# Optimization experiments

Measured on AMD Instinct MI355X. Metric: run time of the kernel, lower is better.

The kernel has to match this reference:

```python
import jax, jax.numpy as jnp
import numpy as np

D = 512; H = 8; HD = D // H; L = 6; QD = 16; MAXLEN = 1000

def _pos_encoding(max_len, d):
    pos = jnp.arange(max_len, dtype=jnp.float32)[:, None]
    div = jnp.exp(jnp.arange(0, d, 2, dtype=jnp.float32) * (-np.log(10000.0) / d))
    pe = jnp.zeros((max_len, d), jnp.float32)
    pe = pe.at[:, 0::2].set(jnp.sin(pos * div))
    pe = pe.at[:, 1::2].set(jnp.cos(pos * div))
    return pe

def _quantum(x, W, b, qwr, qwi, sg, em, mb):
    # QuantumInspiredLayer: classical tanh branch + quantum branch fused by sigmoid gate
    classical = jnp.tanh(x @ W + b)
    qs = x @ sg                          # (B,S,QD) real superposition amplitudes
    ev_r = qs @ qwr                      # complex evolution, real/imag parts kept separate
    ev_i = qs @ qwi
    en_r = ev_r @ em                     # entanglement (real matrix)
    en_i = ev_i @ em
    probs = en_r ** 2 + en_i ** 2        # |entangled|^2, (B,S,QD)
    qout = probs @ mb                    # measurement, (B,S,D)
    fw = jax.nn.sigmoid(jnp.mean(probs, axis=-1, keepdims=True))  # (B,S,1)
    return fw * qout + (1.0 - fw) * classical, probs

def _layer(x, p):
    (Wq, bq, Wk, bk, Wv, bv, Wo, bo,
     qW, qb, qr, qi, qsg, qem, qmb,
     kW, kb, kr, ki, ksg, kem, kmb, g, beta) = p
    B, S, _ = x.shape
    Q = x @ Wq + bq
    K = x @ Wk + bk
    Vv = x @ Wv + bv
    Qq, qp = _quantum(x, qW, qb, qr, qi, qsg, qem, qmb)
    Kq, kp = _quantum(x, kW, kb, kr, ki, ksg, kem, kmb)
    Qf = (0.7 * Q + 0.3 * Qq).reshape(B, S, H, HD).transpose(0, 2, 1, 3)  # (B,H,S,hd)
    Kf = (0.7 * K + 0.3 * Kq).reshape(B, S, H, HD).transpose(0, 2, 1, 3)
    Vh = Vv.reshape(B, S, H, HD).transpose(0, 2, 1, 3)
    scores = jnp.einsum('bhid,bhjd->bhij', Qf, Kf) / np.sqrt(HD).astype(np.float32)
    interf = jnp.einsum('biq,bjq->bij', qp, kp)   # quantum interference term (B,S,S)
    scores = scores + 0.1 * interf[:, None]       # broadcast over heads
    attn = jax.nn.softmax(scores, axis=-1)        # dropout=eval mode (identity)
    ctx = jnp.einsum('bhij,bhjd->bhid', attn, Vh).transpose(0, 2, 1, 3).reshape(B, S, D)
    y = ctx @ Wo + bo + x                         # residual, then LayerNorm
    mu = jnp.mean(y, axis=-1, keepdims=True)
    var = jnp.mean((y - mu) ** 2, axis=-1, keepdims=True)
    y = (y - mu) / jnp.sqrt(var + 1e-5) * g + beta
    return y, attn

def setup_inputs() -> dict:
    key = jax.random.key(0)
    ks = iter(jax.random.split(key, 64))
    def rn(shape, s=0.02):
        return (jax.random.normal(next(ks), shape) * s).astype(jnp.float32)
    B, S, V = 4, 512, 32000
    inp = {
        'text_input': jax.random.randint(next(ks), (B, S), 0, V),
        'visual_input': rn((B, 2048), 1.0),
        'temporal_input': rn((B, 64), 1.0),
        'embed': rn((V, D)),
        'Wvis': rn((2048, D)), 'bvis': jnp.zeros((D,), jnp.float32),
        'Wtemp': rn((64, D)), 'btemp': jnp.zeros((D,), jnp.float32),
        'Wq': rn((L, D, D)), 'bq': jnp.zeros((L, D), jnp.float32),
        'Wk': rn((L, D, D)), 'bk': jnp.zeros((L, D), jnp.float32),
        'Wv': rn((L, D, D)), 'bv': jnp.zeros((L, D), jnp.float32),
        'Wo': rn((L, D, D)), 'bo': jnp.zeros((L, D), jnp.float32),
        'qW': rn((L, D, D)), 'qb': jnp.zeros((L, D), jnp.float32),
        'q_qwr': rn((L, QD, QD), 0.05), 'q_qwi': rn((L, QD, QD), 0.05),
        'q_sg': rn((L, D, QD), 0.05), 'q_em': rn((L, QD, QD), 0.05), 'q_mb': rn((L, QD, D), 0.05),
        'kW': rn((L, D, D)), 'kb': jnp.zeros((L, D), jnp.float32),
        'k_qwr': rn((L, QD, QD), 0.05), 'k_qwi': rn((L, QD, QD), 0.05),
        'k_sg': rn((L, D, QD), 0.05), 'k_em': rn((L, QD, QD), 0.05), 'k_mb': rn((L, QD, D), 0.05),
        'ln_g': jnp.ones((L, D), jnp.float32), 'ln_b': jnp.zeros((L, D), jnp.float32),
        'Ws': rn((D, 64)), 'bs_': jnp.zeros((64,), jnp.float32),
        'Wd': rn((D, 5)), 'bd': jnp.zeros((5,), jnp.float32),
        'We': rn((D, 1)), 'be': jnp.zeros((1,), jnp.float32),
    }
    return inp

def reference(text_input, visual_input, temporal_input, embed, Wvis, bvis, Wtemp, btemp,
              Wq, bq, Wk, bk, Wv, bv, Wo, bo,
              qW, qb, q_qwr, q_qwi, q_sg, q_em, q_mb,
              kW, kb, k_qwr, k_qwi, k_sg, k_em, k_mb,
              ln_g, ln_b, Ws, bs_, Wd, bd, We, be):
    B, S = text_input.shape
    x = (embed[text_input]
         + (visual_input @ Wvis + bvis)[:, None, :]
         + (temporal_input @ Wtemp + btemp)[:, None, :])
    x = x + _pos_encoding(MAXLEN, D)[None, :S, :]
    attns = []
    for l in range(L):
        p = (Wq[l], bq[l], Wk[l], bk[l], Wv[l], bv[l], Wo[l], bo[l],
             qW[l], qb[l], q_qwr[l], q_qwi[l], q_sg[l], q_em[l], q_mb[l],
             kW[l], kb[l], k_qwr[l], k_qwi[l], k_sg[l], k_em[l], k_mb[l],
             ln_g[l], ln_b[l])
        x, a = _layer(x, p)
        attns.append(a)
    pooled = jnp.mean(x, axis=1)  # no attention_mask -> simple mean pool
    skill = jax.nn.sigmoid(pooled @ Ws + bs_)
    diff = jax.nn.softmax(pooled @ Wd + bd, axis=-1)
    eng = jax.nn.sigmoid(pooled @ We + be)
    return skill, diff, eng, x, jnp.stack(attns)
```

## Files before the change

kernel.cpp:

```cpp
#include <hip/hip_runtime.h>
#include <hip/hip_bf16.h>

typedef __attribute__((ext_vector_type(4))) float f32x4;
typedef __attribute__((ext_vector_type(8))) short s16x8;

__device__ __forceinline__ unsigned short f2b(float f) {
  unsigned int u = __float_as_uint(f);
  unsigned int r = (u + 0x7FFFu + ((u >> 16) & 1u)) >> 16;
  return (unsigned short)r;
}
__device__ __forceinline__ float b2f(unsigned short h) {
  return __uint_as_float(((unsigned int)h) << 16);
}
__device__ __forceinline__ void gload16(const void* g, void* l) {
  __builtin_amdgcn_global_load_lds(
      (const __attribute__((address_space(1))) void*)g,
      (__attribute__((address_space(3))) void*)l, 16, 0, 0);
}

enum { MODE_BF16 = 0, MODE_VT = 1, MODE_Y = 2 };
struct OutSpec { void* ptr; int mode; };
struct Outs5 { OutSpec o[5]; };
struct Ptr6 { const float* p[6]; };

template<int BM, int BN, int WGM, int WGN>
__global__ __launch_bounds__(256) void gemm_nt(
    const unsigned short* __restrict__ A, int lda, long long strideA,
    const unsigned short* __restrict__ Bm, int ldb, long long strideB,
    const float* __restrict__ biasBase, int biasStride, int perZ,
    Outs5 outs, const float* __restrict__ resid, int K)
{
  constexpr int BK = 32;
  constexpr int WM = BM / WGM, WN = BN / WGN;
  constexpr int WR = WM / 16, WC = WN / 16;
  constexpr int CHA = BM * BK / 8;
  constexpr int CHB = BN * BK / 8;
  __shared__ unsigned short lds_a[2][BM * BK];
  __shared__ unsigned short lds_b[2][BN * BK];
  const int z = blockIdx.z;
  const int tid = threadIdx.x;
  const int wave = tid >> 6, lane = tid & 63;
  const int l16 = lane & 15, lhi = lane >> 4;
  const int wm = (wave / WGN) * WM, wn = (wave % WGN) * WN;
  const int m0 = blockIdx.x * BM, n0 = blockIdx.y * BN;
  const unsigned short* Ap = A + (long long)z * strideA;
  const unsigned short* Bp = Bm + (long long)z * strideB;

  auto stage = [&](int buf, int k0) {
#pragma unroll
    for (int p = 0; p < CHA / 256; ++p) {
      int t = p * 256 + tid;
      gload16(Ap + (long long)(m0 + (t >> 2)) * lda + k0 + (t & 3) * 8, &lds_a[buf][t * 8]);
    }
    if constexpr (CHA % 256) {
      if (tid < CHA % 256) {
        int t = (CHA / 256) * 256 + tid;
        gload16(Ap + (long long)(m0 + (t >> 2)) * lda + k0 + (t & 3) * 8, &lds_a[buf][t * 8]);
      }
    }
#pragma unroll
    for (int p = 0; p < CHB / 256; ++p) {
      int t = p * 256 + tid;
      gload16(Bp + (long long)(n0 + (t >> 2)) * ldb + k0 + (t & 3) * 8, &lds_b[buf][t * 8]);
    }
    if constexpr (CHB % 256) {
      if (tid < CHB % 256) {
        int t = (CHB / 256) * 256 + tid;
        gload16(Bp + (long long)(n0 + (t >> 2)) * ldb + k0 + (t & 3) * 8, &lds_b[buf][t * 8]);
      }
    }
  };

  f32x4 acc[WR][WC];
#pragma unroll
  for (int r = 0; r < WR; ++r)
#pragma unroll
    for (int c = 0; c < WC; ++c) { f32x4 zz = {0.f, 0.f, 0.f, 0.f}; acc[r][c] = zz; }

  stage(0, 0);
  __syncthreads();
  int cur = 0;
  for (int k0 = 0; k0 < K; k0 += BK) {
    if (k0 + BK < K) stage(cur ^ 1, k0 + BK);
    s16x8 af[WR], bfv[WC];
#pragma unroll
    for (int r = 0; r < WR; ++r)
      af[r] = *(const s16x8*)&lds_a[cur][(wm + r * 16 + l16) * BK + lhi * 8];
#pragma unroll
    for (int c = 0; c < WC; ++c)
      bfv[c] = *(const s16x8*)&lds_b[cur][(wn + c * 16 + l16) * BK + lhi * 8];
#pragma unroll
    for (int r = 0; r < WR; ++r)
#pragma unroll
      for (int c = 0; c < WC; ++c)
        acc[r][c] = __builtin_amdgcn_mfma_f32_16x16x32_bf16(af[r], bfv[c], acc[r][c], 0, 0, 0);
    __syncthreads();
    cur ^= 1;
  }

  OutSpec spec = perZ ? outs.o[z] : outs.o[0];
  const float* bias = biasBase ? (biasBase + (long long)z * biasStride) : nullptr;
#pragma unroll
  for (int r = 0; r < WR; ++r) {
#pragma unroll
    for (int c = 0; c < WC; ++c) {
      int n = n0 + wn + c * 16 + l16;
      int rb = m0 + wm + r * 16 + lhi * 4;
      float bv = bias ? bias[n] : 0.f;
      float vv[4];
#pragma unroll
      for (int j = 0; j < 4; ++j) vv[j] = acc[r][c][j] + bv;
      if (spec.mode == MODE_BF16) {
#pragma unroll
        for (int j = 0; j < 4; ++j)
          ((unsigned short*)spec.ptr)[(long long)(rb + j) * 512 + n] = f2b(vv[j]);
      } else if (spec.mode == MODE_VT) {
        int b = rb >> 9, s = rb & 511;
        ushort4 pk;
        pk.x = f2b(vv[0]); pk.y = f2b(vv[1]); pk.z = f2b(vv[2]); pk.w = f2b(vv[3]);
        *(ushort4*)&((unsigned short*)spec.ptr)[
            (((long long)(b * 8 + (n >> 6))) * 64 + (n & 63)) * 512 + s] = pk;
      } else {
#pragma unroll
        for (int j = 0; j < 4; ++j)
          ((float*)spec.ptr)[(long long)(rb + j) * 512 + n] =
              vv[j] + resid[(long long)(rb + j) * 512 + n];
      }
    }
  }
}

__global__ __launch_bounds__(256, 1) void fused_attn(
    const unsigned short* __restrict__ Qe, const unsigned short* __restrict__ Ke,
    const unsigned short* __restrict__ Vt, float* __restrict__ attn,
    unsigned short* __restrict__ ctx)
{
  __shared__ unsigned short lds[55296];
  const int z = blockIdx.x, rb = blockIdx.y;
  const int m0 = rb * 64;
  const int b = z >> 3, h = z & 7;
  const int tid = threadIdx.x;
  const int w = tid >> 6, lane = tid & 63;
  const int l16 = lane & 15, lhi = lane >> 4;
  const int rx3 = l16 & 3, rx7 = l16 & 7;

#pragma unroll
  for (int p = 0; p < 3; ++p) {
    int t = p * 256 + tid;
    int row = t / 12, c = t % 12;
    gload16(Qe + ((long long)(z * 512 + m0 + row)) * 96 + (c ^ (row & 3)) * 8, &lds[t * 8]);
  }
#pragma unroll
  for (int p = 0; p < 24; ++p) {
    int t = p * 256 + tid;
    int row = t / 12, c = t % 12;
    gload16(Ke + ((long long)(z * 512 + row)) * 96 + (c ^ (row & 3)) * 8, &lds[6144 + t * 8]);
  }
  __syncthreads();

  const unsigned short* Qs = lds;
  const unsigned short* Ks = lds + 6144;
  s16x8 aq[3];
#pragma unroll
  for (int kk = 0; kk < 3; ++kk)
    aq[kk] = *(const s16x8*)&Qs[(w * 16 + l16) * 96 + (kk * 4 + (lhi ^ rx3)) * 8];
  f32x4 acc[32];
#pragma unroll
  for (int c = 0; c < 32; ++c) { f32x4 zz = {0.f, 0.f, 0.f, 0.f}; acc[c] = zz; }
#pragma unroll
  for (int c = 0; c < 32; ++c) {
#pragma unroll
    for (int kk = 0; kk < 3; ++kk) {
      s16x8 bf = *(const s16x8*)&Ks[(c * 16 + l16) * 96 + (kk * 4 + (lhi ^ rx3)) * 8];
      acc[c] = __builtin_amdgcn_mfma_f32_16x16x32_bf16(aq[kk], bf, acc[c], 0, 0, 0);
    }
  }

  float inv[4];
#pragma unroll
  for (int j = 0; j < 4; ++j) {
    float mx = acc[0][j];
#pragma unroll
    for (int c = 1; c < 32; ++c) mx = fmaxf(mx, acc[c][j]);
    mx = fmaxf(mx, __shfl_xor(mx, 1));
    mx = fmaxf(mx, __shfl_xor(mx, 2));
    mx = fmaxf(mx, __shfl_xor(mx, 4));
    mx = fmaxf(mx, __shfl_xor(mx, 8));
    float sum = 0.f;
#pragma unroll
    for (int c = 0; c < 32; ++c) { float e = __expf(acc[c][j] - mx); acc[c][j] = e; sum += e; }
    sum += __shfl_xor(sum, 1);
    sum += __shfl_xor(sum, 2);
    sum += __shfl_xor(sum, 4);
    sum += __shfl_xor(sum, 8);
    inv[j] = 1.f / sum;
  }
  __syncthreads();

#pragma unroll
  for (int p = 0; p < 8; ++p) {
    int t = p * 256 + tid;
    int row = t >> 5, c = t & 31;
    gload16(Vt + (long long)z * 32768 + row * 512 + (c ^ (row & 7)) * 8, &lds[32768 + t * 8]);
  }
  unsigned short* S = lds;
  {
    float* ap = attn + (long long)z * 262144;
#pragma unroll
    for (int j = 0; j < 4; ++j) {
      int row_l = w * 16 + lhi * 4 + j;
      int rs = row_l & 7;
      float* arow = ap + (long long)(m0 + row_l) * 512;
      unsigned short* srow = S + row_l * 512;
#pragma unroll
      for (int c = 0; c < 32; ++c) {
        float p = acc[c][j] * inv[j];
        int col = c * 16 + l16;
        arow[col] = p;
        srow[((col >> 3) ^ rs) * 8 + (col & 7)] = f2b(p);
      }
    }
  }
  __syncthreads();

  const unsigned short* Vl = lds + 32768;
  f32x4 acc2[4];
#pragma unroll
  for (int c2 = 0; c2 < 4; ++c2) { f32x4 zz = {0.f, 0.f, 0.f, 0.f}; acc2[c2] = zz; }
  const int qrow = w * 16 + l16;
#pragma unroll
  for (int kk = 0; kk < 8; ++kk) {
    s16x8 a = *(const s16x8*)&S[qrow * 512 + ((kk * 4 + lhi) ^ rx7) * 8];
#pragma unroll
    for (int c2 = 0; c2 < 4; ++c2) {
      s16x8 bf = *(const s16x8*)&Vl[(c2 * 16 + l16) * 256 + ((kk * 4 + lhi) ^ rx7) * 8];
      acc2[c2] = __builtin_amdgcn_mfma_f32_16x16x32_bf16(a, bf, acc2[c2], 0, 0, 0);
    }
  }
  __syncthreads();
#pragma unroll
  for (int p = 0; p < 8; ++p) {
    int t = p * 256 + tid;
    int row = t >> 5, c = t & 31;
    gload16(Vt + (long long)z * 32768 + row * 512 + 256 + (c ^ (row & 7)) * 8,
            &lds[32768 + t * 8]);
  }
  __syncthreads();
#pragma unroll
  for (int kk = 8; kk < 16; ++kk) {
    s16x8 a = *(const s16x8*)&S[qrow * 512 + ((kk * 4 + lhi) ^ rx7) * 8];
#pragma unroll
    for (int c2 = 0; c2 < 4; ++c2) {
      s16x8 bf = *(const s16x8*)&Vl[(c2 * 16 + l16) * 256 + (((kk - 8) * 4 + lhi) ^ rx7) * 8];
      acc2[c2] = __builtin_amdgcn_mfma_f32_16x16x32_bf16(a, bf, acc2[c2], 0, 0, 0);
    }
  }
#pragma unroll
  for (int c2 = 0; c2 < 4; ++c2) {
#pragma unroll
    for (int j = 0; j < 4; ++j) {
      int row_g = m0 + w * 16 + lhi * 4 + j;
      ctx[((long long)(b * 512 + row_g)) * 512 + h * 64 + c2 * 16 + l16] = f2b(acc2[c2][j]);
    }
  }
}

__global__ __launch_bounds__(256) void wt_k(Ptr6 srcs, unsigned short* __restrict__ wt) {
  __shared__ float tile[32][33];
  int zz = blockIdx.z;
  int l = zz / 6, mat = zz % 6;
  const float* src = srcs.p[mat] + (long long)l * 262144;
  int tx = threadIdx.x, ty = threadIdx.y;
  int n0 = blockIdx.x * 32, k0 = blockIdx.y * 32;
#pragma unroll
  for (int r = 0; r < 4; ++r)
    tile[ty + r * 8][tx] = src[(long long)(k0 + ty + r * 8) * 512 + n0 + tx];
  __syncthreads();
#pragma unroll
  for (int r = 0; r < 4; ++r)
    wt[(long long)zz * 262144 + (long long)(n0 + ty + r * 8) * 512 + k0 + tx] =
        f2b(tile[tx][ty + r * 8]);
}

__global__ __launch_bounds__(256) void prep_k(Ptr6 biases,
    const float* __restrict__ qwr, const float* __restrict__ qwi, const float* __restrict__ qem,
    const float* __restrict__ kwr, const float* __restrict__ kwi, const float* __restrict__ kem,
    float* __restrict__ biasPacked, float* __restrict__ ArAi) {
  int l = blockIdx.x, t = threadIdx.x;
  for (int m = 0; m < 6; ++m)
    for (int d = t; d < 512; d += 256)
      biasPacked[(l * 6 + m) * 512 + d] = biases.p[m][l * 512 + d];
  int i = t >> 4, j = t & 15;
  const float* em0 = qem + l * 256;
  float ar = 0.f, ai = 0.f;
  for (int tt = 0; tt < 16; ++tt) {
    ar += qwr[l * 256 + i * 16 + tt] * em0[tt * 16 + j];
    ai += qwi[l * 256 + i * 16 + tt] * em0[tt * 16 + j];
  }
  ArAi[(l * 4 + 0) * 256 + t] = ar;
  ArAi[(l * 4 + 1) * 256 + t] = ai;
  const float* em1 = kem + l * 256;
  ar = 0.f; ai = 0.f;
  for (int tt = 0; tt < 16; ++tt) {
    ar += kwr[l * 256 + i * 16 + tt] * em1[tt * 16 + j];
    ai += kwi[l * 256 + i * 16 + tt] * em1[tt * 16 + j];
  }
  ArAi[(l * 4 + 2) * 256 + t] = ar;
  ArAi[(l * 4 + 3) * 256 + t] = ai;
}

__global__ __launch_bounds__(512) void vispart_k(const float* __restrict__ vis,
    const float* __restrict__ Wvis, float* __restrict__ part) {
  int b = blockIdx.x, chunk = blockIdx.y, d = threadIdx.x;
  float acc = 0.f;
  for (int k = chunk * 64; k < chunk * 64 + 64; ++k)
    acc += vis[b * 2048 + k] * Wvis[(long long)k * 512 + d];
  part[(b * 32 + chunk) * 512 + d] = acc;
}
__global__ __launch_bounds__(512) void projsum_k(const float* __restrict__ part,
    const float* __restrict__ bvis, const float* __restrict__ temporal,
    const float* __restrict__ Wtemp, const float* __restrict__ btemp, float* __restrict__ proj) {
  int b = blockIdx.x, d = threadIdx.x;
  float acc = bvis[d] + btemp[d];
  for (int c = 0; c < 32; ++c) acc += part[(b * 32 + c) * 512 + d];
  for (int k = 0; k < 64; ++k) acc += temporal[b * 64 + k] * Wtemp[k * 512 + d];
  proj[b * 512 + d] = acc;
}

__global__ __launch_bounds__(512) void embed_k(const int* __restrict__ text,
    const float* __restrict__ emb, const float* __restrict__ proj,
    float* __restrict__ x, unsigned short* __restrict__ xb) {
  int row = blockIdx.x;
  int b = row >> 9, s = row & 511;
  int d = threadIdx.x;
  int tok = text[row];
  float v = emb[(long long)tok * 512 + d] + proj[b * 512 + d];
  float fr = __expf((float)((d >> 1) << 1) * (-9.2103403719761836f / 512.f));
  float ang = (float)s * fr;
  v += (d & 1) ? cosf(ang) : sinf(ang);
  x[(long long)row * 512 + d] = v;
  xb[(long long)row * 512 + d] = f2b(v);
}

__global__ __launch_bounds__(64) void quantum_k(const unsigned short* __restrict__ xb,
    const float* __restrict__ sg_q, const float* __restrict__ sg_k,
    const float* __restrict__ ArAiL, float* __restrict__ qp, float* __restrict__ kp,
    float* __restrict__ fwq, float* __restrict__ fwk) {
  int row = blockIdx.x, side = blockIdx.y, lane = threadIdx.x;
  const float* sg = side ? sg_k : sg_q;
  const float* Ar = ArAiL + side * 512;
  const float* Ai = Ar + 256;
  float acc[16];
#pragma unroll
  for (int j = 0; j < 16; ++j) acc[j] = 0.f;
  s16x8 xv8 = *(const s16x8*)(xb + (long long)row * 512 + lane * 8);
#pragma unroll
  for (int e = 0; e < 8; ++e) {
    float xv = b2f((unsigned short)xv8[e]);
    const float* sgr = sg + (lane * 8 + e) * 16;
#pragma unroll
    for (int j = 0; j < 16; ++j) acc[j] += xv * sgr[j];
  }
#pragma unroll
  for (int s = 32; s; s >>= 1)
#pragma unroll
    for (int j = 0; j < 16; ++j) acc[j] += __shfl_xor(acc[j], s);
  int j = lane & 15;
  float tr = 0.f, ti = 0.f;
#pragma unroll
  for (int t = 0; t < 16; ++t) {
    tr += acc[t] * Ar[t * 16 + j];
    ti += acc[t] * Ai[t * 16 + j];
  }
  float p = tr * tr + ti * ti;
  float ps = p;
#pragma unroll
  for (int s = 1; s < 16; s <<= 1) ps += __shfl_xor(ps, s);
  if (lane < 16) (side ? kp : qp)[row * 16 + lane] = p;
  if (lane == 0) (side ? fwk : fwq)[row] = 1.f / (1.f + __expf(-ps * (1.f / 16.f)));
}

struct FuseP {
  const unsigned short* lin; const unsigned short* cl; const float* qp; const float* fw;
  const float* mb; unsigned short* ext; float sA, sB;
};
struct Fuse2 { FuseP s[2]; };
__global__ __launch_bounds__(512) void fuse_k(Fuse2 fp) {
  FuseP P = fp.s[blockIdx.y];
  int row = blockIdx.x;
  int b = row >> 9, i = row & 511;
  int d = threadIdx.x;
  const float* qpr = P.qp + row * 16;
  float fwv = P.fw[row];
  float qout = 0.f;
#pragma unroll
  for (int t = 0; t < 16; ++t) qout += qpr[t] * P.mb[t * 512 + d];
  float qq = fwv * qout + (1.f - fwv) * tanhf(b2f(P.cl[(long long)row * 512 + d]));
  float val = (0.7f * b2f(P.lin[(long long)row * 512 + d]) + 0.3f * qq) * P.sA;
  int h = d >> 6, dd = d & 63;
  P.ext[(((long long)(b * 8 + h)) * 512 + i) * 96 + dd] = f2b(val);
  if (d < 128) {
    int h2 = d >> 4, j = d & 15;
    P.ext[(((long long)(b * 8 + h2)) * 512 + i) * 96 + 64 + j] = f2b(P.sB * qpr[j]);
  } else if (d < 256) {
    int t2 = d - 128;
    int h2 = t2 >> 4, j = t2 & 15;
    P.ext[(((long long)(b * 8 + h2)) * 512 + i) * 96 + 80 + j] = 0;
  }
}

__global__ __launch_bounds__(256) void ln_k(const float* __restrict__ y,
    const float* __restrict__ g, const float* __restrict__ be,
    float* __restrict__ xo, unsigned short* __restrict__ xb, float* __restrict__ xo2) {
  int wv = threadIdx.x >> 6, lane = threadIdx.x & 63;
  long long row = (long long)blockIdx.x * 4 + wv;
  const float* yr = y + row * 512 + lane * 8;
  f32x4 a = *(const f32x4*)yr, b = *(const f32x4*)(yr + 4);
  float s = a[0] + a[1] + a[2] + a[3] + b[0] + b[1] + b[2] + b[3];
#pragma unroll
  for (int m = 32; m; m >>= 1) s += __shfl_xor(s, m);
  float mu = s * (1.f / 512.f);
  float d[8], vs = 0.f;
#pragma unroll
  for (int j = 0; j < 4; ++j) { d[j] = a[j] - mu; vs += d[j] * d[j]; }
#pragma unroll
  for (int j = 0; j < 4; ++j) { d[4 + j] = b[j] - mu; vs += d[4 + j] * d[4 + j]; }
#pragma unroll
  for (int m = 32; m; m >>= 1) vs += __shfl_xor(vs, m);
  float rstd = rsqrtf(vs * (1.f / 512.f) + 1e-5f);
  f32x4 g0 = *(const f32x4*)(g + lane * 8), g1 = *(const f32x4*)(g + lane * 8 + 4);
  f32x4 b0 = *(const f32x4*)(be + lane * 8), b1 = *(const f32x4*)(be + lane * 8 + 4);
  f32x4 o0, o1; s16x8 ob;
#pragma unroll
  for (int j = 0; j < 4; ++j) { o0[j] = d[j] * rstd * g0[j] + b0[j]; ob[j] = (short)f2b(o0[j]); }
#pragma unroll
  for (int j = 0; j < 4; ++j) { o1[j] = d[4 + j] * rstd * g1[j] + b1[j]; ob[4 + j] = (short)f2b(o1[j]); }
  float* xr = xo + row * 512 + lane * 8;
  *(f32x4*)xr = o0; *(f32x4*)(xr + 4) = o1;
  *(s16x8*)(xb + row * 512 + lane * 8) = ob;
  if (xo2) {
    float* x2 = xo2 + row * 512 + lane * 8;
    *(f32x4*)x2 = o0; *(f32x4*)(x2 + 4) = o1;
  }
}

__global__ __launch_bounds__(512) void poolpart_k(const float* __restrict__ x,
                                                   float* __restrict__ part) {
  int b = blockIdx.x, ch = blockIdx.y, d = threadIdx.x;
  float s = 0.f;
  for (int r = 0; r < 64; ++r) s += x[((long long)(b * 512 + ch * 64 + r)) * 512 + d];
  part[(b * 8 + ch) * 512 + d] = s;
}
__global__ __launch_bounds__(512) void head_k(const float* __restrict__ part,
    const float* __restrict__ Ws, const float* __restrict__ bs,
    const float* __restrict__ Wd, const float* __restrict__ bd,
    const float* __restrict__ We, const float* __restrict__ be, float* __restrict__ out) {
  __shared__ float pooled[512];
  __shared__ float dl[5];
  int b = blockIdx.x, d = threadIdx.x;
  float s = 0.f;
  for (int t = 0; t < 8; ++t) s += part[(b * 8 + t) * 512 + d];
  pooled[d] = s * (1.f / 512.f);
  __syncthreads();
  if (d < 64) {
    float a = bs[d];
    for (int t = 0; t < 512; ++t) a += pooled[t] * Ws[t * 64 + d];
    out[b * 64 + d] = 1.f / (1.f + __expf(-a));
  } else if (d < 69) {
    int j = d - 64;
    float a = bd[j];
    for (int t = 0; t < 512; ++t) a += pooled[t] * Wd[t * 5 + j];
    dl[j] = a;
  } else if (d == 69) {
    float a = be[0];
    for (int t = 0; t < 512; ++t) a += pooled[t] * We[t];
    out[276 + b] = 1.f / (1.f + __expf(-a));
  }
  __syncthreads();
  if (d < 5) {
    float mx = dl[0];
    for (int j = 1; j < 5; ++j) mx = fmaxf(mx, dl[j]);
    float sm = 0.f;
    for (int j = 0; j < 5; ++j) sm += __expf(dl[j] - mx);
    out[256 + b * 5 + d] = __expf(dl[d] - mx) / sm;
  }
}

extern "C" void kernel_launch(void* const* d_in, const int* in_sizes, int n_in,
                              void* d_out, int out_size, void* d_ws, size_t ws_size,
                              hipStream_t stream) {
  (void)in_sizes; (void)n_in; (void)out_size; (void)ws_size;
  const int*   text     = (const int*)  d_in[0];
  const float* visual   = (const float*)d_in[1];
  const float* temporal = (const float*)d_in[2];
  const float* embedw   = (const float*)d_in[3];
  const float* Wvis  = (const float*)d_in[4];  const float* bvis  = (const float*)d_in[5];
  const float* Wtemp = (const float*)d_in[6];  const float* btemp = (const float*)d_in[7];
  const float* Wq = (const float*)d_in[8];   const float* bq = (const float*)d_in[9];
  const float* Wk = (const float*)d_in[10];  const float* bk = (const float*)d_in[11];
  const float* Wv = (const float*)d_in[12];  const float* bv = (const float*)d_in[13];
  const float* Wo = (const float*)d_in[14];  const float* bo = (const float*)d_in[15];
  const float* qW = (const float*)d_in[16];  const float* qb = (const float*)d_in[17];
  const float* q_qwr = (const float*)d_in[18]; const float* q_qwi = (const float*)d_in[19];
  const float* q_sg  = (const float*)d_in[20]; const float* q_em  = (const float*)d_in[21];
  const float* q_mb  = (const float*)d_in[22];
  const float* kW = (const float*)d_in[23];  const float* kb = (const float*)d_in[24];
  const float* k_qwr = (const float*)d_in[25]; const float* k_qwi = (const float*)d_in[26];
  const float* k_sg  = (const float*)d_in[27]; const float* k_em  = (const float*)d_in[28];
  const float* k_mb  = (const float*)d_in[29];
  const float* ln_g = (const float*)d_in[30]; const float* ln_b = (const float*)d_in[31];
  const float* Ws = (const float*)d_in[32];  const float* bs_ = (const float*)d_in[33];
  const float* Wd = (const float*)d_in[34];  const float* bd = (const float*)d_in[35];
  const float* We = (const float*)d_in[36];  const float* be = (const float*)d_in[37];
  float* out = (float*)d_out;

  char* w = (char*)d_ws;
  auto alloc = [&](size_t bytes) {
    char* p = w;
    w += (bytes + 255) & ~(size_t)255;
    return p;
  };
  float* ws_x   = (float*)alloc(2048ll * 512 * 4);
  unsigned short* ws_xb = (unsigned short*)alloc(2048ll * 512 * 2);
  unsigned short* ws_Wt = (unsigned short*)alloc(36ll * 262144 * 2);
  float* ws_bias = (float*)alloc(6ll * 6 * 512 * 4);
  float* ws_ArAi = (float*)alloc(6ll * 1024 * 4);
  float* ws_proj = (float*)alloc(4ll * 512 * 4);
  float* ws_vp   = (float*)alloc(4ll * 32 * 512 * 4);
  unsigned short* ws_Q  = (unsigned short*)alloc(2048ll * 512 * 2);
  unsigned short* ws_K  = (unsigned short*)alloc(2048ll * 512 * 2);
  unsigned short* ws_Cq = (unsigned short*)alloc(2048ll * 512 * 2);
  unsigned short* ws_Ck = (unsigned short*)alloc(2048ll * 512 * 2);
  float* ws_qp   = (float*)alloc(2048ll * 16 * 4);
  float* ws_kp   = (float*)alloc(2048ll * 16 * 4);
  float* ws_fwq  = (float*)alloc(2048ll * 4);
  float* ws_fwk  = (float*)alloc(2048ll * 4);
  unsigned short* ws_Vt   = (unsigned short*)alloc(2048ll * 512 * 2);
  unsigned short* ws_Qext = (unsigned short*)alloc(4ll * 8 * 512 * 96 * 2);
  unsigned short* ws_Kext = (unsigned short*)alloc(4ll * 8 * 512 * 96 * 2);
  unsigned short* ws_ctx  = (unsigned short*)alloc(2048ll * 512 * 2);
  float* ws_y    = (float*)alloc(2048ll * 512 * 4);

  Ptr6 wsrc = {{Wq, Wk, Wv, qW, kW, Wo}};
  wt_k<<<dim3(16, 16, 36), dim3(32, 8), 0, stream>>>(wsrc, ws_Wt);
  Ptr6 bsrc = {{bq, bk, bv, qb, kb, bo}};
  prep_k<<<dim3(6), dim3(256), 0, stream>>>(bsrc, q_qwr, q_qwi, q_em, k_qwr, k_qwi, k_em,
                                            ws_bias, ws_ArAi);
  vispart_k<<<dim3(4, 32), dim3(512), 0, stream>>>(visual, Wvis, ws_vp);
  projsum_k<<<dim3(4), dim3(512), 0, stream>>>(ws_vp, bvis, temporal, Wtemp, btemp, ws_proj);
  embed_k<<<dim3(2048), dim3(512), 0, stream>>>(text, embedw, ws_proj, ws_x, ws_xb);

  const long long ATTN_OFF = 280ll + 1048576ll;
  for (int l = 0; l < 6; ++l) {
    const unsigned short* WtL = ws_Wt + (long long)l * 6 * 262144;
    const float* biasL = ws_bias + (long long)l * 6 * 512;

    Outs5 o5{};
    o5.o[0] = { ws_Q, MODE_BF16 };  o5.o[1] = { ws_K, MODE_BF16 };
    o5.o[2] = { ws_Vt, MODE_VT };   o5.o[3] = { ws_Cq, MODE_BF16 };
    o5.o[4] = { ws_Ck, MODE_BF16 };
    gemm_nt<128, 64, 2, 2><<<dim3(16, 8, 5), 256, 0, stream>>>(
        ws_xb, 512, 0ll, WtL, 512, 262144ll, biasL, 512, 1, o5, nullptr, 512);

    quantum_k<<<dim3(2048, 2), 64, 0, stream>>>(ws_xb, q_sg + l * 8192, k_sg + l * 8192,
        ws_ArAi + l * 1024, ws_qp, ws_kp, ws_fwq, ws_fwk);

    Fuse2 f2{};
    f2.s[0] = { ws_Q, ws_Cq, ws_qp, ws_fwq, q_mb + l * 8192, ws_Qext, 0.125f, 0.1f };
    f2.s[1] = { ws_K, ws_Ck, ws_kp, ws_fwk, k_mb + l * 8192, ws_Kext, 1.0f, 1.0f };
    fuse_k<<<dim3(2048, 2), dim3(512), 0, stream>>>(f2);

    fused_attn<<<dim3(32, 8), 256, 0, stream>>>(
        ws_Qext, ws_Kext, ws_Vt, out + ATTN_OFF + (long long)l * 8388608, ws_ctx);

    Outs5 oy{};
    oy.o[0] = { ws_y, MODE_Y };
    gemm_nt<64, 64, 2, 2><<<dim3(32, 8, 1), 256, 0, stream>>>(
        ws_ctx, 512, 0ll, WtL + 5 * 262144, 512, 0ll, biasL + 5 * 512, 0, 0, oy, ws_x, 512);

    ln_k<<<dim3(512), dim3(256), 0, stream>>>(ws_y, ln_g + l * 512, ln_b + l * 512,
        ws_x, ws_xb, (l == 5) ? (out + 280) : nullptr);
  }

  poolpart_k<<<dim3(4, 8), dim3(512), 0, stream>>>(ws_x, ws_vp);
  head_k<<<dim3(4), dim3(512), 0, stream>>>(ws_vp, Ws, bs_, Wd, bd, We, be, out);
}
```

Baseline: 521.9 us.

## Fuse quantum and fuse kernels, move residual add into LayerNorm, enlarge QKV tile

Merges the per-row quantum probability kernel and the Q/K extension fuse kernel into one kernel that keeps probs and gate values in shared memory, which removes a launch and the intermediate global buffers. The output projection GEMM now writes bf16 without the residual, and the residual add moves into the LayerNorm kernel, halving the output write size. The QKV GEMM tile grows to 128x128. Rounding the projection output to bf16 before the residual slightly reduces precision, and the larger tile launches fewer blocks.

```diff
diff --git a/kernel.cpp b/kernel.cpp
--- a/kernel.cpp
+++ b/kernel.cpp
@@ -18,7 +18,7 @@
       (__attribute__((address_space(3))) void*)l, 16, 0, 0);
 }
 
-enum { MODE_BF16 = 0, MODE_VT = 1, MODE_Y = 2 };
+enum { MODE_BF16 = 0, MODE_VT = 1 };
 struct OutSpec { void* ptr; int mode; };
 struct Outs5 { OutSpec o[5]; };
 struct Ptr6 { const float* p[6]; };
@@ -28,7 +28,7 @@
     const unsigned short* __restrict__ A, int lda, long long strideA,
     const unsigned short* __restrict__ Bm, int ldb, long long strideB,
     const float* __restrict__ biasBase, int biasStride, int perZ,
-    Outs5 outs, const float* __restrict__ resid, int K)
+    Outs5 outs, int K)
 {
   constexpr int BK = 32;
   constexpr int WM = BM / WGM, WN = BN / WGN;
@@ -114,17 +114,12 @@
 #pragma unroll
         for (int j = 0; j < 4; ++j)
           ((unsigned short*)spec.ptr)[(long long)(rb + j) * 512 + n] = f2b(vv[j]);
-      } else if (spec.mode == MODE_VT) {
+      } else {
         int b = rb >> 9, s = rb & 511;
         ushort4 pk;
         pk.x = f2b(vv[0]); pk.y = f2b(vv[1]); pk.z = f2b(vv[2]); pk.w = f2b(vv[3]);
         *(ushort4*)&((unsigned short*)spec.ptr)[
             (((long long)(b * 8 + (n >> 6))) * 64 + (n & 63)) * 512 + s] = pk;
-      } else {
-#pragma unroll
-        for (int j = 0; j < 4; ++j)
-          ((float*)spec.ptr)[(long long)(rb + j) * 512 + n] =
-              vv[j] + resid[(long long)(rb + j) * 512 + n];
       }
     }
   }
@@ -261,6 +256,85 @@
     for (int j = 0; j < 4; ++j) {
       int row_g = m0 + w * 16 + lhi * 4 + j;
       ctx[((long long)(b * 512 + row_g)) * 512 + h * 64 + c2 * 16 + l16] = f2b(acc2[c2][j]);
+    }
+  }
+}
+
+__global__ __launch_bounds__(512) void qfuse_k(
+    const unsigned short* __restrict__ xb,
+    const unsigned short* __restrict__ Qlin, const unsigned short* __restrict__ Klin,
+    const unsigned short* __restrict__ Cq, const unsigned short* __restrict__ Ck,
+    const float* __restrict__ sg_q, const float* __restrict__ sg_k,
+    const float* __restrict__ ArAiL,
+    const float* __restrict__ mb_q, const float* __restrict__ mb_k,
+    unsigned short* __restrict__ Qext, unsigned short* __restrict__ Kext)
+{
+  __shared__ float probs[2][16];
+  __shared__ float fwv[2];
+  const int row = blockIdx.x;
+  const int tid = threadIdx.x;
+  const int w = tid >> 6, lane = tid & 63;
+
+  if (w < 2) {
+    const float* sg = w ? sg_k : sg_q;
+    const float* Ar = ArAiL + w * 512;
+    const float* Ai = Ar + 256;
+    float acc[16];
+#pragma unroll
+    for (int j = 0; j < 16; ++j) acc[j] = 0.f;
+    s16x8 xv8 = *(const s16x8*)(xb + (long long)row * 512 + lane * 8);
+#pragma unroll
+    for (int e = 0; e < 8; ++e) {
+      float xv = b2f((unsigned short)xv8[e]);
+      const float* sgr = sg + (lane * 8 + e) * 16;
+#pragma unroll
+      for (int j = 0; j < 16; ++j) acc[j] += xv * sgr[j];
+    }
+#pragma unroll
+    for (int s = 32; s; s >>= 1)
+#pragma unroll
+      for (int j = 0; j < 16; ++j) acc[j] += __shfl_xor(acc[j], s);
+    int j = lane & 15;
+    float tr = 0.f, ti = 0.f;
+#pragma unroll
+    for (int t = 0; t < 16; ++t) {
+      tr += acc[t] * Ar[t * 16 + j];
+      ti += acc[t] * Ai[t * 16 + j];
+    }
+    float p = tr * tr + ti * ti;
+    float ps = p;
+#pragma unroll
+    for (int s = 1; s < 16; s <<= 1) ps += __shfl_xor(ps, s);
+    if (lane < 16) probs[w][lane] = p;
+    if (lane == 0) fwv[w] = 1.f / (1.f + __expf(-ps * (1.f / 16.f)));
+  }
+  __syncthreads();
+
+  const int d = tid;
+  const int b = row >> 9, i = row & 511;
+  const int h = d >> 6, dd = d & 63;
+#pragma unroll
+  for (int side = 0; side < 2; ++side) {
+    const unsigned short* lin = side ? Klin : Qlin;
+    const unsigned short* cl  = side ? Ck : Cq;
+    const float* mb = side ? mb_k : mb_q;
+    unsigned short* ext = side ? Kext : Qext;
+    float sA = side ? 1.0f : 0.125f;
+    float sB = side ? 1.0f : 0.1f;
+    float fw = fwv[side];
+    float qout = 0.f;
+#pragma unroll
+    for (int t = 0; t < 16; ++t) qout += probs[side][t] * mb[t * 512 + d];
+    float qq = fw * qout + (1.f - fw) * tanhf(b2f(cl[(long long)row * 512 + d]));
+    float val = (0.7f * b2f(lin[(long long)row * 512 + d]) + 0.3f * qq) * sA;
+    ext[(((long long)(b * 8 + h)) * 512 + i) * 96 + dd] = f2b(val);
+    if (d < 128) {
+      int h2 = d >> 4, jj = d & 15;
+      ext[(((long long)(b * 8 + h2)) * 512 + i) * 96 + 64 + jj] = f2b(sB * probs[side][jj]);
+    } else if (d < 256) {
+      int t2 = d - 128;
+      int h2 = t2 >> 4, jj = t2 & 15;
+      ext[(((long long)(b * 8 + h2)) * 512 + i) * 96 + 80 + jj] = 0;
     }
   }
 }
@@ -342,89 +416,25 @@
   xb[(long long)row * 512 + d] = f2b(v);
 }
 
-__global__ __launch_bounds__(64) void quantum_k(const unsigned short* __restrict__ xb,
-    const float* __restrict__ sg_q, const float* __restrict__ sg_k,
-    const float* __restrict__ ArAiL, float* __restrict__ qp, float* __restrict__ kp,
-    float* __restrict__ fwq, float* __restrict__ fwk) {
-  int row = blockIdx.x, side = blockIdx.y, lane = threadIdx.x;
-  const float* sg = side ? sg_k : sg_q;
-  const float* Ar = ArAiL + side * 512;
-  const float* Ai = Ar + 256;
-  float acc[16];
-#pragma unroll
-  for (int j = 0; j < 16; ++j) acc[j] = 0.f;
-  s16x8 xv8 = *(const s16x8*)(xb + (long long)row * 512 + lane * 8);
-#pragma unroll
-  for (int e = 0; e < 8; ++e) {
-    float xv = b2f((unsigned short)xv8[e]);
-    const float* sgr = sg + (lane * 8 + e) * 16;
-#pragma unroll
-    for (int j = 0; j < 16; ++j) acc[j] += xv * sgr[j];
-  }
-#pragma unroll
-  for (int s = 32; s; s >>= 1)
-#pragma unroll
-    for (int j = 0; j < 16; ++j) acc[j] += __shfl_xor(acc[j], s);
-  int j = lane & 15;
-  float tr = 0.f, ti = 0.f;
-#pragma unroll
-  for (int t = 0; t < 16; ++t) {
-    tr += acc[t] * Ar[t * 16 + j];
-    ti += acc[t] * Ai[t * 16 + j];
-  }
-  float p = tr * tr + ti * ti;
-  float ps = p;
-#pragma unroll
-  for (int s = 1; s < 16; s <<= 1) ps += __shfl_xor(ps, s);
-  if (lane < 16) (side ? kp : qp)[row * 16 + lane] = p;
-  if (lane == 0) (side ? fwk : fwq)[row] = 1.f / (1.f + __expf(-ps * (1.f / 16.f)));
-}
-
-struct FuseP {
-  const unsigned short* lin; const unsigned short* cl; const float* qp; const float* fw;
-  const float* mb; unsigned short* ext; float sA, sB;
-};
-struct Fuse2 { FuseP s[2]; };
-__global__ __launch_bounds__(512) void fuse_k(Fuse2 fp) {
-  FuseP P = fp.s[blockIdx.y];
-  int row = blockIdx.x;
-  int b = row >> 9, i = row & 511;
-  int d = threadIdx.x;
-  const float* qpr = P.qp + row * 16;
-  float fwv = P.fw[row];
-  float qout = 0.f;
-#pragma unroll
-  for (int t = 0; t < 16; ++t) qout += qpr[t] * P.mb[t * 512 + d];
-  float qq = fwv * qout + (1.f - fwv) * tanhf(b2f(P.cl[(long long)row * 512 + d]));
-  float val = (0.7f * b2f(P.lin[(long long)row * 512 + d]) + 0.3f * qq) * P.sA;
-  int h = d >> 6, dd = d & 63;
-  P.ext[(((long long)(b * 8 + h)) * 512 + i) * 96 + dd] = f2b(val);
-  if (d < 128) {
-    int h2 = d >> 4, j = d & 15;
-    P.ext[(((long long)(b * 8 + h2)) * 512 + i) * 96 + 64 + j] = f2b(P.sB * qpr[j]);
-  } else if (d < 256) {
-    int t2 = d - 128;
-    int h2 = t2 >> 4, j = t2 & 15;
-    P.ext[(((long long)(b * 8 + h2)) * 512 + i) * 96 + 80 + j] = 0;
-  }
-}
-
-__global__ __launch_bounds__(256) void ln_k(const float* __restrict__ y,
+__global__ __launch_bounds__(256) void ln_k(const unsigned short* __restrict__ go,
     const float* __restrict__ g, const float* __restrict__ be,
-    float* __restrict__ xo, unsigned short* __restrict__ xb, float* __restrict__ xo2) {
+    float* __restrict__ x, unsigned short* __restrict__ xb, float* __restrict__ xo2) {
   int wv = threadIdx.x >> 6, lane = threadIdx.x & 63;
   long long row = (long long)blockIdx.x * 4 + wv;
-  const float* yr = y + row * 512 + lane * 8;
-  f32x4 a = *(const f32x4*)yr, b = *(const f32x4*)(yr + 4);
-  float s = a[0] + a[1] + a[2] + a[3] + b[0] + b[1] + b[2] + b[3];
+  s16x8 gv = *(const s16x8*)(go + row * 512 + lane * 8);
+  float* xr = x + row * 512 + lane * 8;
+  f32x4 a = *(const f32x4*)xr, bq = *(const f32x4*)(xr + 4);
+  float f[8], s = 0.f;
+#pragma unroll
+  for (int j = 0; j < 4; ++j) { f[j] = b2f((unsigned short)gv[j]) + a[j]; s += f[j]; }
+#pragma unroll
+  for (int j = 0; j < 4; ++j) { f[4 + j] = b2f((unsigned short)gv[4 + j]) + bq[j]; s += f[4 + j]; }
 #pragma unroll
   for (int m = 32; m; m >>= 1) s += __shfl_xor(s, m);
   float mu = s * (1.f / 512.f);
   float d[8], vs = 0.f;
 #pragma unroll
-  for (int j = 0; j < 4; ++j) { d[j] = a[j] - mu; vs += d[j] * d[j]; }
-#pragma unroll
-  for (int j = 0; j < 4; ++j) { d[4 + j] = b[j] - mu; vs += d[4 + j] * d[4 + j]; }
+  for (int j = 0; j < 8; ++j) { d[j] = f[j] - mu; vs += d[j] * d[j]; }
 #pragma unroll
   for (int m = 32; m; m >>= 1) vs += __shfl_xor(vs, m);
   float rstd = rsqrtf(vs * (1.f / 512.f) + 1e-5f);
@@ -435,7 +445,6 @@
   for (int j = 0; j < 4; ++j) { o0[j] = d[j] * rstd * g0[j] + b0[j]; ob[j] = (short)f2b(o0[j]); }
 #pragma unroll
   for (int j = 0; j < 4; ++j) { o1[j] = d[4 + j] * rstd * g1[j] + b1[j]; ob[4 + j] = (short)f2b(o1[j]); }
-  float* xr = xo + row * 512 + lane * 8;
   *(f32x4*)xr = o0; *(f32x4*)(xr + 4) = o1;
   *(s16x8*)(xb + row * 512 + lane * 8) = ob;
   if (xo2) {
@@ -531,15 +540,11 @@
   unsigned short* ws_K  = (unsigned short*)alloc(2048ll * 512 * 2);
   unsigned short* ws_Cq = (unsigned short*)alloc(2048ll * 512 * 2);
   unsigned short* ws_Ck = (unsigned short*)alloc(2048ll * 512 * 2);
-  float* ws_qp   = (float*)alloc(2048ll * 16 * 4);
-  float* ws_kp   = (float*)alloc(2048ll * 16 * 4);
-  float* ws_fwq  = (float*)alloc(2048ll * 4);
-  float* ws_fwk  = (float*)alloc(2048ll * 4);
   unsigned short* ws_Vt   = (unsigned short*)alloc(2048ll * 512 * 2);
   unsigned short* ws_Qext = (unsigned short*)alloc(4ll * 8 * 512 * 96 * 2);
   unsigned short* ws_Kext = (unsigned short*)alloc(4ll * 8 * 512 * 96 * 2);
   unsigned short* ws_ctx  = (unsigned short*)alloc(2048ll * 512 * 2);
-  float* ws_y    = (float*)alloc(2048ll * 512 * 4);
+  unsigned short* ws_go   = (unsigned short*)alloc(2048ll * 512 * 2);
 
   Ptr6 wsrc = {{Wq, Wk, Wv, qW, kW, Wo}};
   wt_k<<<dim3(16, 16, 36), dim3(32, 8), 0, stream>>>(wsrc, ws_Wt);
@@ -559,26 +564,22 @@
     o5.o[0] = { ws_Q, MODE_BF16 };  o5.o[1] = { ws_K, MODE_BF16 };
     o5.o[2] = { ws_Vt, MODE_VT };   o5.o[3] = { ws_Cq, MODE_BF16 };
     o5.o[4] = { ws_Ck, MODE_BF16 };
-    gemm_nt<128, 64, 2, 2><<<dim3(16, 8, 5), 256, 0, stream>>>(
-        ws_xb, 512, 0ll, WtL, 512, 262144ll, biasL, 512, 1, o5, nullptr, 512);
-
-    quantum_k<<<dim3(2048, 2), 64, 0, stream>>>(ws_xb, q_sg + l * 8192, k_sg + l * 8192,
-        ws_ArAi + l * 1024, ws_qp, ws_kp, ws_fwq, ws_fwk);
-
-    Fuse2 f2{};
-    f2.s[0] = { ws_Q, ws_Cq, ws_qp, ws_fwq, q_mb + l * 8192, ws_Qext, 0.125f, 0.1f };
-    f2.s[1] = { ws_K, ws_Ck, ws_kp, ws_fwk, k_mb + l * 8192, ws_Kext, 1.0f, 1.0f };
-    fuse_k<<<dim3(2048, 2), dim3(512), 0, stream>>>(f2);
+    gemm_nt<128, 128, 2, 2><<<dim3(16, 4, 5), 256, 0, stream>>>(
+        ws_xb, 512, 0ll, WtL, 512, 262144ll, biasL, 512, 1, o5, 512);
+
+    qfuse_k<<<dim3(2048), dim3(512), 0, stream>>>(
+        ws_xb, ws_Q, ws_K, ws_Cq, ws_Ck, q_sg + l * 8192, k_sg + l * 8192,
+        ws_ArAi + l * 1024, q_mb + l * 8192, k_mb + l * 8192, ws_Qext, ws_Kext);
 
     fused_attn<<<dim3(32, 8), 256, 0, stream>>>(
         ws_Qext, ws_Kext, ws_Vt, out + ATTN_OFF + (long long)l * 8388608, ws_ctx);
 
     Outs5 oy{};
-    oy.o[0] = { ws_y, MODE_Y };
+    oy.o[0] = { ws_go, MODE_BF16 };
     gemm_nt<64, 64, 2, 2><<<dim3(32, 8, 1), 256, 0, stream>>>(
-        ws_ctx, 512, 0ll, WtL + 5 * 262144, 512, 0ll, biasL + 5 * 512, 0, 0, oy, ws_x, 512);
-
-    ln_k<<<dim3(512), dim3(256), 0, stream>>>(ws_y, ln_g + l * 512, ln_b + l * 512,
+        ws_ctx, 512, 0ll, WtL + 5 * 262144, 512, 0ll, biasL + 5 * 512, 0, 0, oy, 512);
+
+    ln_k<<<dim3(512), dim3(256), 0, stream>>>(ws_go, ln_g + l * 512, ln_b + l * 512,
         ws_x, ws_xb, (l == 5) ? (out + 280) : nullptr);
   }
 
```

After: 533.8 us. 1.02x slower.
